# Performance work log

Measured on AMD Instinct MI355X. Metric: run time of the kernel, lower is better.

## Reference

```python
import jax, jax.numpy as jnp
import numpy as np

DIM = 1024
N_HEAD = 16
HEAD_DIM = DIM // N_HEAD
B, T = 4, 2048
NEG = -1e9


def setup_inputs() -> dict:
    key = jax.random.key(0)
    ks = jax.random.split(key, 5)
    x = jax.random.normal(ks[0], (B, T, DIM), dtype=jnp.float32)
    # additive causal mask, broadcast over batch and heads
    causal = jnp.triu(jnp.full((T, T), NEG, dtype=jnp.float32), k=1)
    mask = causal[None, None, :, :]  # [1,1,T,T]
    s = 1.0 / np.sqrt(DIM)
    wq = jax.random.normal(ks[1], (DIM, DIM), dtype=jnp.float32) * s
    wk = jax.random.normal(ks[2], (DIM, DIM), dtype=jnp.float32) * s
    wv = jax.random.normal(ks[3], (DIM, DIM), dtype=jnp.float32) * s
    wo = jax.random.normal(ks[4], (DIM, DIM), dtype=jnp.float32) * s
    return {"x": x, "mask": mask, "wq": wq, "wk": wk, "wv": wv, "wo": wo}


def reference(x, mask, wq, wk, wv, wo):
    Bn, Tn, C = x.shape
    # torch nn.Linear(dim,dim,bias=False): y = x @ W^T
    q = (x @ wq.T).reshape(Bn, Tn, N_HEAD, HEAD_DIM).transpose(0, 2, 1, 3)  # [B,H,T,D]
    k = (x @ wk.T).reshape(Bn, Tn, N_HEAD, HEAD_DIM).transpose(0, 2, 1, 3)
    v = (x @ wv.T).reshape(Bn, Tn, N_HEAD, HEAD_DIM).transpose(0, 2, 1, 3)
    scale = 1.0 / np.sqrt(HEAD_DIM).astype(np.float32)
    attn = jnp.einsum('bhqd,bhkd->bhqk', q, k) * scale  # [B,H,T,T]
    attn = attn + mask
    attn = jax.nn.softmax(attn, axis=-1)
    out = jnp.einsum('bhqk,bhkd->bhqd', attn, v)  # [B,H,T,D]
    out = out.transpose(0, 2, 1, 3).reshape(Bn, Tn, C)
    return out @ wo.T
```

## Files before the change

### kernel.cpp

```cpp
#include <hip/hip_runtime.h>
#include <hip/hip_bf16.h>

typedef __attribute__((ext_vector_type(8))) short short8;
typedef __attribute__((ext_vector_type(4))) short short4v;
typedef __attribute__((ext_vector_type(4))) float float4v;

#define DIM   1024
#define NH    16
#define HD    64
#define BSZ   4
#define TSZ   2048
#define BT    (BSZ*TSZ)

#define SBIAS 24.0f

#define PIDX(row, col) ((((row)*64 + (col)) ^ (((row)&7) << 3)))

typedef const __attribute__((address_space(1))) void* gptr_t;
typedef __attribute__((address_space(3))) void* lptr_t;

__device__ __forceinline__ short f2bs(float x) {
    __hip_bfloat16 h = __float2bfloat16(x);
    return __builtin_bit_cast(short, h);
}

__global__ __launch_bounds__(256) void cvt_kernel(
    const float* __restrict__ x,  const float* __restrict__ wq,
    const float* __restrict__ wk, const float* __restrict__ wv,
    const float* __restrict__ wo,
    __hip_bfloat16* __restrict__ xb,  __hip_bfloat16* __restrict__ wqb,
    __hip_bfloat16* __restrict__ wkb, __hip_bfloat16* __restrict__ wvb,
    __hip_bfloat16* __restrict__ wob)
{
    int bid = blockIdx.x;
    const float* src; __hip_bfloat16* dst; int base;
    if (bid < 8192) { src = x; dst = xb; base = bid; }
    else {
        int wsel = (bid - 8192) >> 10;
        base = (bid - 8192) & 1023;
        src = (wsel == 0) ? wq : (wsel == 1) ? wk : (wsel == 2) ? wv : wo;
        dst = (wsel == 0) ? wqb : (wsel == 1) ? wkb : (wsel == 2) ? wvb : wob;
    }
    size_t off = (size_t)base * 1024 + threadIdx.x * 4;
    float4v v = *(const float4v*)(src + off);
    short4v o;
    o[0] = f2bs(v[0]); o[1] = f2bs(v[1]); o[2] = f2bs(v[2]); o[3] = f2bs(v[3]);
    *(short4v*)((short*)dst + off) = o;
}

__global__ __launch_bounds__(256, 2) void qkv_gemm(
    const __hip_bfloat16* __restrict__ xb,
    const __hip_bfloat16* __restrict__ wqb,
    const __hip_bfloat16* __restrict__ wkb,
    const __hip_bfloat16* __restrict__ wvb,
    __hip_bfloat16* __restrict__ Qt,
    __hip_bfloat16* __restrict__ Kb,
    __hip_bfloat16* __restrict__ Vt)
{
    __shared__ __hip_bfloat16 smA[128*64];
    __shared__ __hip_bfloat16 smB[3][128*64];

    const int tid = threadIdx.x;
    const int wid = tid >> 6, lane = tid & 63;
    const int quad = lane >> 4, l15 = lane & 15;
    const int l7 = l15 & 7;
    const int m0 = blockIdx.x * 128, n0 = blockIdx.y * 128;
    const int wm = (wid >> 1) * 64, wn = (wid & 1) * 64;
    const int wm0 = m0 + wm, wn0 = n0 + wn;
    const int srow = tid >> 3;
    const int scol = ((tid & 7) ^ (srow & 7)) * 8;
    const float qscale = 0.1803368801111204f;

    const __hip_bfloat16* gA0 = xb  + (size_t)(m0 + srow) * DIM + scol;
    const __hip_bfloat16* gBq = wqb + (size_t)(n0 + srow) * DIM + scol;
    const __hip_bfloat16* gBk = wkb + (size_t)(n0 + srow) * DIM + scol;
    const __hip_bfloat16* gBv = wvb + (size_t)(n0 + srow) * DIM + scol;

    float4v acc[3][4][4];
#pragma unroll
    for (int z = 0; z < 3; z++)
#pragma unroll
        for (int i = 0; i < 4; i++)
#pragma unroll
            for (int j = 0; j < 4; j++)
#pragma unroll
                for (int r = 0; r < 4; r++) acc[z][i][j][r] = 0.0f;

    for (int kc = 0; kc < DIM; kc += 64) {
        __syncthreads();
#pragma unroll
        for (int j = 0; j < 4; j++) {
            __builtin_amdgcn_global_load_lds((gptr_t)(gA0 + (size_t)(j*32)*DIM + kc),
                (lptr_t)(smA + j*2048 + tid*8), 16, 0, 0);
            __builtin_amdgcn_global_load_lds((gptr_t)(gBq + (size_t)(j*32)*DIM + kc),
                (lptr_t)(&smB[0][0] + j*2048 + tid*8), 16, 0, 0);
            __builtin_amdgcn_global_load_lds((gptr_t)(gBk + (size_t)(j*32)*DIM + kc),
                (lptr_t)(&smB[1][0] + j*2048 + tid*8), 16, 0, 0);
            __builtin_amdgcn_global_load_lds((gptr_t)(gBv + (size_t)(j*32)*DIM + kc),
                (lptr_t)(&smB[2][0] + j*2048 + tid*8), 16, 0, 0);
        }
        __syncthreads();

#pragma unroll
        for (int s = 0; s < 2; s++) {
            short8 a[4];
#pragma unroll
            for (int mb = 0; mb < 4; mb++)
                a[mb] = *(const short8*)(smA + (wm + mb*16 + l15)*64 + ((s*4 + quad) ^ l7)*8);
#pragma unroll
            for (int z = 0; z < 3; z++) {
                short8 b[4];
#pragma unroll
                for (int nb = 0; nb < 4; nb++)
                    b[nb] = *(const short8*)(&smB[z][0] + (wn + nb*16 + l15)*64 + ((s*4 + quad) ^ l7)*8);
#pragma unroll
                for (int mb = 0; mb < 4; mb++)
#pragma unroll
                    for (int nb = 0; nb < 4; nb++)
                        acc[z][mb][nb] = __builtin_amdgcn_mfma_f32_16x16x32_bf16(
                            a[mb], b[nb], acc[z][mb][nb], 0, 0, 0);
            }
        }
    }

    {
        const int h = wn0 >> 6;
#pragma unroll
        for (int mb = 0; mb < 4; mb++) {
            int m = wm0 + mb*16 + quad*4;
            int bb = m >> 11, t0 = m & 2047;
#pragma unroll
            for (int nb = 0; nb < 4; nb++) {
                int d = nb*16 + l15;
                short4v pq, pv;
                pq[0] = f2bs(acc[0][mb][nb][0] * qscale); pq[1] = f2bs(acc[0][mb][nb][1] * qscale);
                pq[2] = f2bs(acc[0][mb][nb][2] * qscale); pq[3] = f2bs(acc[0][mb][nb][3] * qscale);
                pv[0] = f2bs(acc[2][mb][nb][0]); pv[1] = f2bs(acc[2][mb][nb][1]);
                pv[2] = f2bs(acc[2][mb][nb][2]); pv[3] = f2bs(acc[2][mb][nb][3]);
                size_t base = (size_t)((bb*NH + h)*HD + d)*TSZ + t0;
                *(short4v*)(Qt + base) = pq;
                *(short4v*)(Vt + base) = pv;
            }
        }
    }
#pragma unroll
    for (int mb = 0; mb < 4; mb++)
#pragma unroll
        for (int r = 0; r < 4; r++) {
            int m = wm0 + mb*16 + quad*4 + r;
            int bb = m >> 11, t = m & 2047;
#pragma unroll
            for (int nb = 0; nb < 4; nb++) {
                int n = wn0 + nb*16 + l15;
                int h = n >> 6, d = n & 63;
                Kb[(size_t)((bb*NH + h)*TSZ + t)*HD + d] =
                    __float2bfloat16(acc[1][mb][nb][r]);
            }
        }
}

__global__ __launch_bounds__(256, 2) void attn(
    const __hip_bfloat16* __restrict__ Qt,
    const __hip_bfloat16* __restrict__ Kb,
    const __hip_bfloat16* __restrict__ Vt,
    __hip_bfloat16* __restrict__ Ob)
{
    __shared__ __hip_bfloat16 smK[64*64];
    __shared__ __hip_bfloat16 smV[64*64];
    __shared__ __hip_bfloat16 Pl[4][32*64];

    const int qperm[16] = {15,14,13,12,8,9,10,11,4,5,6,7,3,2,1,0};
    const int bh = blockIdx.x;
    const int qt = qperm[blockIdx.y];
    const int q0 = qt * 128;
    const int tid = threadIdx.x;
    const int wid = tid >> 6, lane = tid & 63;
    const int quad = lane >> 4, l15 = lane & 15;
    const int l7 = l15 & 7;
    const int q0w = q0 + wid * 32;

    const __hip_bfloat16* Qp = Qt + (size_t)bh * HD * TSZ;
    const __hip_bfloat16* Kp = Kb + (size_t)bh * TSZ * HD;
    const __hip_bfloat16* Vp = Vt + (size_t)bh * HD * TSZ;
    __hip_bfloat16* P = &Pl[wid][0];

    const int srow = tid >> 3;
    const int scol = ((tid & 7) ^ (srow & 7)) * 8;

    short8 bq[2][2];
#pragma unroll
    for (int nt = 0; nt < 2; nt++)
#pragma unroll
        for (int c = 0; c < 2; c++) {
            short8 v;
#pragma unroll
            for (int j = 0; j < 8; j++)
                v[j] = ((const short*)Qp)[(size_t)(c*32 + quad*8 + j)*TSZ
                                          + (q0w + nt*16 + l15)];
            bq[nt][c] = v;
        }

    float lsum[2] = {0.f, 0.f};
    float4v ot[4][2];
#pragma unroll
    for (int mt = 0; mt < 4; mt++)
#pragma unroll
        for (int nt = 0; nt < 2; nt++)
#pragma unroll
            for (int r = 0; r < 4; r++) ot[mt][nt][r] = 0.f;

    const int ntb = 2*qt + 2;
    for (int it = 0; it < ntb; ++it) {
        const int k0 = it * 64;

        __syncthreads();
#pragma unroll
        for (int c = 0; c < 2; c++) {
            __builtin_amdgcn_global_load_lds(
                (gptr_t)(Kp + (size_t)(k0 + srow + 32*c)*HD + scol),
                (lptr_t)(smK + tid*8 + c*2048), 16, 0, 0);
            __builtin_amdgcn_global_load_lds(
                (gptr_t)(Vp + (size_t)(srow + 32*c)*TSZ + k0 + scol),
                (lptr_t)(smV + tid*8 + c*2048), 16, 0, 0);
        }
        __syncthreads();

        if (k0 > q0w + 31) continue;

        float4v st[4][2];
#pragma unroll
        for (int mt = 0; mt < 4; mt++)
#pragma unroll
            for (int nt = 0; nt < 2; nt++)
#pragma unroll
                for (int r = 0; r < 4; r++) st[mt][nt][r] = -SBIAS;
#pragma unroll
        for (int c = 0; c < 2; c++)
#pragma unroll
            for (int mt = 0; mt < 4; mt++) {
                short8 ak = *(const short8*)(smK + (mt*16 + l15)*64 + ((c*4 + quad) ^ l7)*8);
                st[mt][0] = __builtin_amdgcn_mfma_f32_16x16x32_bf16(ak, bq[0][c], st[mt][0], 0, 0, 0);
                st[mt][1] = __builtin_amdgcn_mfma_f32_16x16x32_bf16(ak, bq[1][c], st[mt][1], 0, 0, 0);
            }

        if (k0 + 63 > q0w) {
#pragma unroll
            for (int mt = 0; mt < 4; mt++) {
                if (k0 + mt*16 + 15 > q0w) {
#pragma unroll
                    for (int nt = 0; nt < 2; nt++) {
                        int qn = q0w + nt*16 + l15;
#pragma unroll
                        for (int r = 0; r < 4; r++) {
                            int kg = k0 + mt*16 + quad*4 + r;
                            if (kg > qn) st[mt][nt][r] = -1e30f;
                        }
                    }
                }
            }
        }

#pragma unroll
        for (int nt = 0; nt < 2; nt++) {
            float rs = 0.f;
#pragma unroll
            for (int mt = 0; mt < 4; mt++) {
                float p0 = exp2f(st[mt][nt][0]);
                float p1 = exp2f(st[mt][nt][1]);
                float p2 = exp2f(st[mt][nt][2]);
                float p3 = exp2f(st[mt][nt][3]);
                rs += (p0 + p1) + (p2 + p3);
                short4v pk;
                pk[0] = f2bs(p0); pk[1] = f2bs(p1);
                pk[2] = f2bs(p2); pk[3] = f2bs(p3);
                *(short4v*)(P + PIDX(nt*16 + l15, mt*16 + quad*4)) = pk;
            }
            lsum[nt] += rs;
        }

        short8 bp[2][2];
#pragma unroll
        for (int nt = 0; nt < 2; nt++)
#pragma unroll
            for (int c2 = 0; c2 < 2; c2++)
                bp[nt][c2] = *(const short8*)(P + PIDX(nt*16 + l15, c2*32 + quad*8));

#pragma unroll
        for (int c2 = 0; c2 < 2; c2++)
#pragma unroll
            for (int mt = 0; mt < 4; mt++) {
                short8 av = *(const short8*)(smV + (mt*16 + l15)*64 + ((c2*4 + quad) ^ l7)*8);
                ot[mt][0] = __builtin_amdgcn_mfma_f32_16x16x32_bf16(av, bp[0][c2], ot[mt][0], 0, 0, 0);
                ot[mt][1] = __builtin_amdgcn_mfma_f32_16x16x32_bf16(av, bp[1][c2], ot[mt][1], 0, 0, 0);
            }
    }

    const int b = bh >> 4, h = bh & 15;
#pragma unroll
    for (int nt = 0; nt < 2; nt++) {
        float ls = lsum[nt];
        ls += __shfl_xor(ls, 16);
        ls += __shfl_xor(ls, 32);
        const float inv = 1.0f / ls;
        const int qn = q0w + nt*16 + l15;
        const size_t rowbase = (size_t)((b*TSZ + qn)*NH + h) * HD;
#pragma unroll
        for (int mt = 0; mt < 4; mt++) {
            short4v pk;
            pk[0] = f2bs(ot[mt][nt][0] * inv); pk[1] = f2bs(ot[mt][nt][1] * inv);
            pk[2] = f2bs(ot[mt][nt][2] * inv); pk[3] = f2bs(ot[mt][nt][3] * inv);
            *(short4v*)(Ob + rowbase + mt*16 + quad*4) = pk;
        }
    }
}

__global__ __launch_bounds__(256) void out_gemm(
    const __hip_bfloat16* __restrict__ A,
    const __hip_bfloat16* __restrict__ w,
    float* __restrict__ out)
{
    __shared__ __hip_bfloat16 smA[2][128*64];
    __shared__ __hip_bfloat16 smB[2][128*64];

    const int tid = threadIdx.x;
    const int wid = tid >> 6, lane = tid & 63;
    const int quad = lane >> 4, l15 = lane & 15;
    const int l7 = l15 & 7;
    const int m0 = blockIdx.x * 128, n0 = blockIdx.y * 128;
    const int wm = (wid >> 1) * 64, wn = (wid & 1) * 64;
    const int wm0 = m0 + wm, wn0 = n0 + wn;
    const int srow = tid >> 3;
    const int scol = ((tid & 7) ^ (srow & 7)) * 8;

    const __hip_bfloat16* gA0 = A + (size_t)(m0 + srow) * DIM + scol;
    const __hip_bfloat16* gB0 = w + (size_t)(n0 + srow) * DIM + scol;

    float4v acc[4][4];
#pragma unroll
    for (int i = 0; i < 4; i++)
#pragma unroll
        for (int j = 0; j < 4; j++)
#pragma unroll
            for (int r = 0; r < 4; r++) acc[i][j][r] = 0.0f;

#pragma unroll
    for (int j = 0; j < 4; j++) {
        __builtin_amdgcn_global_load_lds((gptr_t)(gA0 + (size_t)(j*32)*DIM),
            (lptr_t)(&smA[0][0] + j*2048 + tid*8), 16, 0, 0);
        __builtin_amdgcn_global_load_lds((gptr_t)(gB0 + (size_t)(j*32)*DIM),
            (lptr_t)(&smB[0][0] + j*2048 + tid*8), 16, 0, 0);
    }

    int cur = 0;
    for (int kc = 0; kc < DIM; kc += 64) {
        __syncthreads();

        if (kc + 64 < DIM) {
            const int kn = kc + 64;
#pragma unroll
            for (int j = 0; j < 4; j++) {
                __builtin_amdgcn_global_load_lds((gptr_t)(gA0 + (size_t)(j*32)*DIM + kn),
                    (lptr_t)(&smA[cur^1][0] + j*2048 + tid*8), 16, 0, 0);
                __builtin_amdgcn_global_load_lds((gptr_t)(gB0 + (size_t)(j*32)*DIM + kn),
                    (lptr_t)(&smB[cur^1][0] + j*2048 + tid*8), 16, 0, 0);
            }
        }

        const __hip_bfloat16* sA = &smA[cur][0];
        const __hip_bfloat16* sB = &smB[cur][0];
#pragma unroll
        for (int s = 0; s < 2; s++) {
            short8 a[4], b[4];
#pragma unroll
            for (int mb = 0; mb < 4; mb++)
                a[mb] = *(const short8*)(sA + (wm + mb*16 + l15)*64 + ((s*4 + quad) ^ l7)*8);
#pragma unroll
            for (int nb = 0; nb < 4; nb++)
                b[nb] = *(const short8*)(sB + (wn + nb*16 + l15)*64 + ((s*4 + quad) ^ l7)*8);
#pragma unroll
            for (int mb = 0; mb < 4; mb++)
#pragma unroll
                for (int nb = 0; nb < 4; nb++)
                    acc[mb][nb] = __builtin_amdgcn_mfma_f32_16x16x32_bf16(
                        a[mb], b[nb], acc[mb][nb], 0, 0, 0);
        }
        cur ^= 1;
    }

#pragma unroll
    for (int mb = 0; mb < 4; mb++)
#pragma unroll
        for (int nb = 0; nb < 4; nb++)
#pragma unroll
            for (int r = 0; r < 4; r++) {
                int m = wm0 + mb*16 + quad*4 + r;
                int n = wn0 + nb*16 + l15;
                out[(size_t)m*DIM + n] = acc[mb][nb][r];
            }
}

extern "C" void kernel_launch(void* const* d_in, const int* in_sizes, int n_in,
                              void* d_out, int out_size, void* d_ws, size_t ws_size,
                              hipStream_t stream) {
    const float* x  = (const float*)d_in[0];
    const float* wq = (const float*)d_in[2];
    const float* wk = (const float*)d_in[3];
    const float* wv = (const float*)d_in[4];
    const float* wo = (const float*)d_in[5];
    float* out = (float*)d_out;

    char* ws = (char*)d_ws;
    const size_t MB = (size_t)1024 * 1024;
    __hip_bfloat16* Qt  = (__hip_bfloat16*)(ws);
    __hip_bfloat16* Kb  = (__hip_bfloat16*)(ws + 16*MB);
    __hip_bfloat16* Vt  = (__hip_bfloat16*)(ws + 32*MB);
    __hip_bfloat16* xb  = (__hip_bfloat16*)(ws + 48*MB);
    __hip_bfloat16* Ob  = (__hip_bfloat16*)(ws + 48*MB);
    __hip_bfloat16* wqb = (__hip_bfloat16*)(ws + 64*MB);
    __hip_bfloat16* wkb = (__hip_bfloat16*)(ws + 66*MB);
    __hip_bfloat16* wvb = (__hip_bfloat16*)(ws + 68*MB);
    __hip_bfloat16* wob = (__hip_bfloat16*)(ws + 70*MB);

    dim3 blk(256);
    cvt_kernel<<<dim3(8192 + 4*1024), blk, 0, stream>>>(
        x, wq, wk, wv, wo, xb, wqb, wkb, wvb, wob);
    qkv_gemm<<<dim3(BT/128, DIM/128), blk, 0, stream>>>(
        xb, wqb, wkb, wvb, Qt, Kb, Vt);
    attn<<<dim3(BSZ*NH, 16), blk, 0, stream>>>(Qt, Kb, Vt, Ob);
    out_gemm<<<dim3(BT/128, DIM/128), blk, 0, stream>>>(Ob, wob, out);
}
```

Baseline: 246.6 us.

## Double-buffer QKV GEMM shared tiles with K=32 prefetch pipeline

```diff
diff --git a/kernel.cpp b/kernel.cpp
--- a/kernel.cpp
+++ b/kernel.cpp
@@ -57,19 +57,19 @@
     __hip_bfloat16* __restrict__ Kb,
     __hip_bfloat16* __restrict__ Vt)
 {
-    __shared__ __hip_bfloat16 smA[128*64];
-    __shared__ __hip_bfloat16 smB[3][128*64];
+    __shared__ __hip_bfloat16 smA[2][128*32];
+    __shared__ __hip_bfloat16 smB[2][3][128*32];
 
     const int tid = threadIdx.x;
     const int wid = tid >> 6, lane = tid & 63;
     const int quad = lane >> 4, l15 = lane & 15;
-    const int l7 = l15 & 7;
     const int m0 = blockIdx.x * 128, n0 = blockIdx.y * 128;
     const int wm = (wid >> 1) * 64, wn = (wid & 1) * 64;
     const int wm0 = m0 + wm, wn0 = n0 + wn;
-    const int srow = tid >> 3;
-    const int scol = ((tid & 7) ^ (srow & 7)) * 8;
     const float qscale = 0.1803368801111204f;
+
+    const int srow = tid >> 2;
+    const int scol = ((tid & 3) ^ ((tid >> 3) & 3)) * 8;
 
     const __hip_bfloat16* gA0 = xb  + (size_t)(m0 + srow) * DIM + scol;
     const __hip_bfloat16* gBq = wqb + (size_t)(n0 + srow) * DIM + scol;
@@ -86,41 +86,64 @@
 #pragma unroll
                 for (int r = 0; r < 4; r++) acc[z][i][j][r] = 0.0f;
 
-    for (int kc = 0; kc < DIM; kc += 64) {
+    const int ra[4] = { wm + 0*16 + l15, wm + 1*16 + l15, wm + 2*16 + l15, wm + 3*16 + l15 };
+    const int rb[4] = { wn + 0*16 + l15, wn + 1*16 + l15, wn + 2*16 + l15, wn + 3*16 + l15 };
+
+#pragma unroll
+    for (int j = 0; j < 2; j++) {
+        __builtin_amdgcn_global_load_lds((gptr_t)(gA0 + (size_t)(j*64)*DIM),
+            (lptr_t)(&smA[0][0] + j*2048 + tid*8), 16, 0, 0);
+        __builtin_amdgcn_global_load_lds((gptr_t)(gBq + (size_t)(j*64)*DIM),
+            (lptr_t)(&smB[0][0][0] + j*2048 + tid*8), 16, 0, 0);
+        __builtin_amdgcn_global_load_lds((gptr_t)(gBk + (size_t)(j*64)*DIM),
+            (lptr_t)(&smB[0][1][0] + j*2048 + tid*8), 16, 0, 0);
+        __builtin_amdgcn_global_load_lds((gptr_t)(gBv + (size_t)(j*64)*DIM),
+            (lptr_t)(&smB[0][2][0] + j*2048 + tid*8), 16, 0, 0);
+    }
+
+    int cur = 0;
+    for (int kc = 0; kc < DIM; kc += 32) {
         __syncthreads();
-#pragma unroll
-        for (int j = 0; j < 4; j++) {
-            __builtin_amdgcn_global_load_lds((gptr_t)(gA0 + (size_t)(j*32)*DIM + kc),
-                (lptr_t)(smA + j*2048 + tid*8), 16, 0, 0);
-            __builtin_amdgcn_global_load_lds((gptr_t)(gBq + (size_t)(j*32)*DIM + kc),
-                (lptr_t)(&smB[0][0] + j*2048 + tid*8), 16, 0, 0);
-            __builtin_amdgcn_global_load_lds((gptr_t)(gBk + (size_t)(j*32)*DIM + kc),
-                (lptr_t)(&smB[1][0] + j*2048 + tid*8), 16, 0, 0);
-            __builtin_amdgcn_global_load_lds((gptr_t)(gBv + (size_t)(j*32)*DIM + kc),
-                (lptr_t)(&smB[2][0] + j*2048 + tid*8), 16, 0, 0);
-        }
-        __syncthreads();
-
-#pragma unroll
-        for (int s = 0; s < 2; s++) {
-            short8 a[4];
+
+        if (kc + 32 < DIM) {
+            const int kn = kc + 32;
+#pragma unroll
+            for (int j = 0; j < 2; j++) {
+                __builtin_amdgcn_global_load_lds((gptr_t)(gA0 + (size_t)(j*64)*DIM + kn),
+                    (lptr_t)(&smA[cur^1][0] + j*2048 + tid*8), 16, 0, 0);
+                __builtin_amdgcn_global_load_lds((gptr_t)(gBq + (size_t)(j*64)*DIM + kn),
+                    (lptr_t)(&smB[cur^1][0][0] + j*2048 + tid*8), 16, 0, 0);
+                __builtin_amdgcn_global_load_lds((gptr_t)(gBk + (size_t)(j*64)*DIM + kn),
+                    (lptr_t)(&smB[cur^1][1][0] + j*2048 + tid*8), 16, 0, 0);
+                __builtin_amdgcn_global_load_lds((gptr_t)(gBv + (size_t)(j*64)*DIM + kn),
+                    (lptr_t)(&smB[cur^1][2][0] + j*2048 + tid*8), 16, 0, 0);
+            }
+        }
+
+        const __hip_bfloat16* sA = &smA[cur][0];
+        short8 a[4];
+#pragma unroll
+        for (int mb = 0; mb < 4; mb++) {
+            int r = ra[mb];
+            a[mb] = *(const short8*)(sA + r*32 + ((quad ^ ((r >> 1) & 3)))*8);
+        }
+#pragma unroll
+        for (int z = 0; z < 3; z++) {
+            const __hip_bfloat16* sB = &smB[cur][z][0];
+            short8 b[4];
+#pragma unroll
+            for (int nb = 0; nb < 4; nb++) {
+                int r = rb[nb];
+                b[nb] = *(const short8*)(sB + r*32 + ((quad ^ ((r >> 1) & 3)))*8);
+            }
 #pragma unroll
             for (int mb = 0; mb < 4; mb++)
-                a[mb] = *(const short8*)(smA + (wm + mb*16 + l15)*64 + ((s*4 + quad) ^ l7)*8);
-#pragma unroll
-            for (int z = 0; z < 3; z++) {
-                short8 b[4];
 #pragma unroll
                 for (int nb = 0; nb < 4; nb++)
-                    b[nb] = *(const short8*)(&smB[z][0] + (wn + nb*16 + l15)*64 + ((s*4 + quad) ^ l7)*8);
-#pragma unroll
-                for (int mb = 0; mb < 4; mb++)
-#pragma unroll
-                    for (int nb = 0; nb < 4; nb++)
-                        acc[z][mb][nb] = __builtin_amdgcn_mfma_f32_16x16x32_bf16(
-                            a[mb], b[nb], acc[z][mb][nb], 0, 0, 0);
-            }
-        }
+                    acc[z][mb][nb] = __builtin_amdgcn_mfma_f32_16x16x32_bf16(
+                        a[mb], b[nb], acc[z][mb][nb], 0, 0, 0);
+        }
+        cur ^= 1;
     }
 
     {
```

After: 250.4 us. About the same (+1.5%).
